# Kernel optimization log

Measured on AMD Instinct MI355X. Metric: run time of the kernel, lower is better.

Reference implementation:

```python
import jax, jax.numpy as jnp
import numpy as np

B, S, H, MODES = 16, 8192, 256, 16

def setup_inputs() -> dict:
    key = jax.random.key(0)
    k1, k2, k3 = jax.random.split(key, 3)
    x = jax.random.normal(k1, (B, S, H), dtype=jnp.float32)
    # complex weights ~ 0.02 * randn (real and imag parts kept as floats)
    w_real = jax.random.normal(k2, (H, H, MODES), dtype=jnp.float32) * 0.02
    w_imag = jax.random.normal(k3, (H, H, MODES), dtype=jnp.float32) * 0.02
    return {"x": x, "w_real": w_real, "w_imag": w_imag}

def reference(x, w_real, w_imag):
    batch, seq_len, hidden = x.shape
    x_ft = jnp.fft.rfft(x, axis=1)                      # [B, F, H] complex64, F = S//2 + 1
    m = min(MODES, x_ft.shape[1])
    w = (w_real + 1j * w_imag)[:, :, :m]                # [H, K, m]
    # batched complex matmul over the kept modes (replaces per-mode loop)
    out_modes = jnp.einsum('bmh,hkm->bmk', x_ft[:, :m, :], w)
    out_ft = jnp.zeros_like(x_ft).at[:, :m, :].set(out_modes)
    y = jnp.fft.irfft(out_ft, n=seq_len, axis=1)        # [B, S, H] float32
    return jax.nn.gelu(y, approximate=False)            # torch nn.GELU default = exact erf
```

## Files before the change

kernel.cpp:

```cpp
#include <hip/hip_runtime.h>
#include <math.h>

#define BB 16
#define SS 8192
#define HH 256
#define MM 16
#define NV 2049
#define VC 8
#define CPB 4
#define DNC 65
#define SCH 16
#define SNC 129


__device__ __forceinline__ void gl_lds16(const float* g, float* l) {
    __builtin_amdgcn_global_load_lds(
        (const __attribute__((address_space(1))) void*)g,
        (__attribute__((address_space(3))) void*)l, 16, 0, 0);
}

__global__ __launch_bounds__(256) void k_twiddle(float* __restrict__ T) {
    int idx = blockIdx.x * 256 + threadIdx.x;
    if (idx >= NV * MM) return;
    int v = idx >> 4, k = idx & 15;
    int r = (k * v) & (SS - 1);
    float th = (float)r * (6.28318530717958647692f / (float)SS);
    float sn, cn;
    sincosf(th, &sn, &cn);
    T[v * 32 + 2 * k]     = cn;
    T[v * 32 + 2 * k + 1] = sn;
}

__global__ __launch_bounds__(256) void k_wt(const float* __restrict__ wr,
                                            const float* __restrict__ wi,
                                            float* __restrict__ Wtr,
                                            float* __restrict__ Wti) {
    __shared__ float lds[4096 + 256];
    const int h = blockIdx.x, t = threadIdx.x;
    const float* src = (blockIdx.y == 0 ? wr : wi) + (size_t)h * 4096;
    float* dst = (blockIdx.y == 0 ? Wtr : Wti);
#pragma unroll
    for (int j = 0; j < 16; j++) {
        int i = j * 256 + t;
        lds[i + (i >> 4)] = src[i];
    }
    __syncthreads();
#pragma unroll
    for (int m = 0; m < 16; m++) {
        int i = t * 16 + m;
        dst[(size_t)m * (HH * HH) + (size_t)h * HH + t] = lds[i + (i >> 4)];
    }
}

__device__ __forceinline__ float fast_gelu(float y) {
    float x  = fabsf(y) * 0.70710678118654752f;
    float t  = __builtin_amdgcn_rcpf(fmaf(0.3275911f, x, 1.0f));
    float e  = __expf(-x * x);
    float p  = fmaf(fmaf(fmaf(fmaf(1.061405429f, t, -1.453152027f), t,
                   1.421413741f), t, -0.284496736f), t, 0.254829592f) * t;
    float erfabs = fmaf(-p, e, 1.0f);
    return fmaf(0.5f * fabsf(y), erfabs, 0.5f * y);
}

__global__ __launch_bounds__(256) void k_dft(const float* __restrict__ x,
                                             const float* __restrict__ T,
                                             float* __restrict__ Xp) {
    const int b = blockIdx.y, bx = blockIdx.x, t = threadIdx.x;
    const int w = t >> 6;
    const float* xb = x + (size_t)b * SS * HH;

    float cs[MM], sn[MM];
#pragma unroll
    for (int k = 0; k < MM; k++) { cs[k] = 0.f; sn[k] = 0.f; }

    __shared__ float lds[2][4 * VC * HH];

    if (bx == 64) {
        float x0 = xb[t];
        float x2 = xb[(size_t)(SS / 2) * HH + t];
#pragma unroll
        for (int j = 0; j < 8; j++) {
            cs[2 * j]     = x0 + x2;
            cs[2 * j + 1] = x0 - x2;
        }
    } else {
        const int c0 = bx * CPB;

        auto stage = [&](int c, int buf) {
            int v0 = 1 + VC * c;
            const float* bases[4] = {
                xb + (size_t)v0 * HH,
                xb + (size_t)(SS / 2 - v0 - (VC - 1)) * HH,
                xb + (size_t)(SS / 2 + v0) * HH,
                xb + (size_t)(SS - v0 - (VC - 1)) * HH };
#pragma unroll
            for (int s = 0; s < 4; s++)
#pragma unroll
                for (int q = 0; q < 2; q++)
                    gl_lds16(bases[s] + q * 1024 + t * 4,
                             &lds[buf][s * 2048 + q * 1024 + w * 256]);
        };

        auto compute = [&](int c, int buf) {
            int v0 = 1 + VC * c;
            const float* L = &lds[buf][0];
#pragma unroll
            for (int i = 0; i < VC; i++) {
                int v = v0 + i;
                float x0 = L[0 * 2048 + i * 256 + t];
                float x2 = L[1 * 2048 + (VC - 1 - i) * 256 + t];
                float x3 = L[2 * 2048 + i * 256 + t];
                float x1 = L[3 * 2048 + (VC - 1 - i) * 256 + t];
                float hf = (v == SS / 4) ? 0.5f : 1.0f;
                float u = (x0 + x1) * hf, d = (x0 - x1) * hf;
                float ww = (x2 + x3) * hf, e = (x3 - x2) * hf;
                float upw = u + ww, umw = u - ww, dpe = d + e, dme = d - e;
                const float4* tw4 = (const float4*)(T + (size_t)v * 32);
#pragma unroll
                for (int j = 0; j < 8; j++) {
                    float4 tt = tw4[j];
                    cs[2 * j]     = fmaf(tt.x, upw, cs[2 * j]);
                    sn[2 * j]     = fmaf(tt.y, dpe, sn[2 * j]);
                    cs[2 * j + 1] = fmaf(tt.z, umw, cs[2 * j + 1]);
                    sn[2 * j + 1] = fmaf(tt.w, dme, sn[2 * j + 1]);
                }
            }
        };

        stage(c0, 0);
        for (int j = 0; j < CPB; j++) {
            if (j < CPB - 1) {
                stage(c0 + j + 1, (j + 1) & 1);
                asm volatile("s_waitcnt vmcnt(8)" ::: "memory");
            } else {
                asm volatile("s_waitcnt vmcnt(0)" ::: "memory");
            }
            __builtin_amdgcn_sched_barrier(0);
            __builtin_amdgcn_s_barrier();
            compute(c0 + j, j & 1);
            __builtin_amdgcn_s_barrier();
        }
    }

    size_t base = ((size_t)(b * DNC + bx) * MM) * (2 * HH) + t;
#pragma unroll
    for (int k = 0; k < MM; k++) {
        Xp[base + (size_t)k * (2 * HH)]      = cs[k];
        Xp[base + (size_t)k * (2 * HH) + HH] = sn[k];
    }
}

__global__ __launch_bounds__(256) void k_reduce(const float* __restrict__ Xp,
                                                float* __restrict__ Xs) {
    const int t = blockIdx.x * 256 + threadIdx.x;
    const int INNER = MM * 2 * HH;
    int idx4 = t * 4;
    int inner = idx4 & (INNER - 1);
    int b = idx4 >> 13;
    const float* src = Xp + ((size_t)b * DNC) * INNER + inner;
    float4 s = make_float4(0.f, 0.f, 0.f, 0.f);
#pragma unroll 5
    for (int p = 0; p < DNC; p++) {
        float4 v = *(const float4*)(src + (size_t)p * INNER);
        s.x += v.x; s.y += v.y; s.z += v.z; s.w += v.w;
    }
    *(float4*)(Xs + idx4) = s;
}

__global__ __launch_bounds__(256) void k_mix2(const float* __restrict__ Xs,
                                              const float* __restrict__ Wtr,
                                              const float* __restrict__ Wti,
                                              float* __restrict__ AB) {
    const int m = blockIdx.x, b = blockIdx.y, t = threadIdx.x;
    __shared__ float xr_s[HH], xs_s[HH];
    size_t xbase = (((size_t)b * MM + m) * 2) * HH;
    xr_s[t] = Xs[xbase + t];
    xs_s[t] = Xs[xbase + HH + t];
    __syncthreads();

    const float* wr_m = Wtr + (size_t)m * (HH * HH);
    const float* wi_m = Wti + (size_t)m * (HH * HH);
    float re = 0.f, im = 0.f;
#pragma unroll 8
    for (int h = 0; h < HH; h++) {
        float a  = wr_m[(size_t)h * HH + t];
        float bw = wi_m[(size_t)h * HH + t];
        float xr = xr_s[h];
        float xs = xs_s[h];
        re = fmaf(xr, a, re);  re = fmaf(xs, bw, re);
        im = fmaf(xr, bw, im); im = fmaf(-xs, a, im);
    }
    float scale = (m == 0 ? 1.f : 2.f) / (float)SS;
    size_t o = (((size_t)b * MM + m) * 2) * HH + t;
    AB[o]      = scale * re;
    AB[o + HH] = -scale * im;
}

__global__ __launch_bounds__(256) void k_synth(const float* __restrict__ AB,
                                               const float* __restrict__ T,
                                               float* __restrict__ out) {
    const int c = blockIdx.x, b = blockIdx.y, h = threadIdx.x;
    float a[MM], bc[MM];
#pragma unroll
    for (int k = 0; k < MM; k++) {
        size_t o = (((size_t)b * MM + k) * 2) * HH + h;
        a[k]  = AB[o];
        bc[k] = AB[o + HH];
    }
    const int nv = (c == SNC - 1) ? 1 : SCH;
    const int v0 = c * SCH;
    float* ob = out + (size_t)b * SS * HH + h;

#pragma unroll 2
    for (int i = 0; i < nv; i++) {
        int v = v0 + i;
        const float4* tw4 = (const float4*)(T + (size_t)v * 32);
        float Pe = 0.f, Po = 0.f, Qe = 0.f, Qo = 0.f;
#pragma unroll
        for (int j = 0; j < 8; j++) {
            float4 t = tw4[j];
            Pe = fmaf(a[2 * j],      t.x, Pe);
            Qe = fmaf(bc[2 * j],     t.y, Qe);
            Po = fmaf(a[2 * j + 1],  t.z, Po);
            Qo = fmaf(bc[2 * j + 1], t.w, Qo);
        }
        float Pp = Pe + Po, Pm = Pe - Po, Qp = Qe + Qo, Qm = Qe - Qo;
        ob[(size_t)v * HH]                        = fast_gelu(Pp + Qp);
        ob[(size_t)(SS / 2 - v) * HH]             = fast_gelu(Pm - Qm);
        ob[(size_t)(SS / 2 + v) * HH]             = fast_gelu(Pm + Qm);
        ob[(size_t)((SS - v) & (SS - 1)) * HH]    = fast_gelu(Pp - Qp);
    }
}

extern "C" void kernel_launch(void* const* d_in, const int* in_sizes, int n_in,
                              void* d_out, int out_size, void* d_ws, size_t ws_size,
                              hipStream_t stream) {
    const float* x   = (const float*)d_in[0];
    const float* w_r = (const float*)d_in[1];
    const float* w_i = (const float*)d_in[2];
    float* out = (float*)d_out;
    float* ws  = (float*)d_ws;

    float* T   = ws;
    float* AB  = ws + 262144;
    float* Xs  = ws + 393216;
    float* Xp  = out;
    float* Wtr = out + (size_t)16 * 1024 * 1024;
    float* Wti = out + (size_t)17 * 1024 * 1024;

    hipLaunchKernelGGL(k_twiddle, dim3((NV * MM + 255) / 256), dim3(256), 0, stream, T);
    hipLaunchKernelGGL(k_wt,     dim3(HH, 2), dim3(256), 0, stream, w_r, w_i, Wtr, Wti);
    hipLaunchKernelGGL(k_dft,    dim3(DNC, BB), dim3(256), 0, stream, x, T, Xp);
    hipLaunchKernelGGL(k_reduce, dim3(BB * MM * 2 * HH / 1024), dim3(256), 0, stream, Xp, Xs);
    hipLaunchKernelGGL(k_mix2,   dim3(MM, BB), dim3(256), 0, stream, Xs, Wtr, Wti, AB);
    hipLaunchKernelGGL(k_synth,  dim3(SNC, BB), dim3(256), 0, stream, AB, T, out);
}
```

Baseline: 117.0 us.

## Fuse precompute kernels, fold partial reduce into mix, triple-buffer DFT loads

Merges the twiddle and weight-transpose kernels into a single launch, and moves the partial-sum reduction into the mode-mixing kernel so the separate reduce kernel and its intermediate buffer go away. The DFT kernel switches to smaller chunks (VC 4) with more chunks per block and a three-deep LDS ring buffer, which halves the number of partial blocks per batch. The intent is to cut launch overhead and intermediate traffic. The trade-off is fewer DFT blocks (33x16), which lowers parallelism, and a mix kernel that now does a strided partial sum itself.

After: 111.2 us. -4.9%, faster.

```diff
diff --git a/kernel.cpp b/kernel.cpp
--- a/kernel.cpp
+++ b/kernel.cpp
@@ -6,9 +6,9 @@
 #define HH 256
 #define MM 16
 #define NV 2049
-#define VC 8
-#define CPB 4
-#define DNC 65
+#define VC 4
+#define CPB 16
+#define DNC 33
 #define SCH 16
 #define SNC 129
 
@@ -19,36 +19,39 @@
         (__attribute__((address_space(3))) void*)l, 16, 0, 0);
 }
 
-__global__ __launch_bounds__(256) void k_twiddle(float* __restrict__ T) {
-    int idx = blockIdx.x * 256 + threadIdx.x;
-    if (idx >= NV * MM) return;
-    int v = idx >> 4, k = idx & 15;
-    int r = (k * v) & (SS - 1);
-    float th = (float)r * (6.28318530717958647692f / (float)SS);
-    float sn, cn;
-    sincosf(th, &sn, &cn);
-    T[v * 32 + 2 * k]     = cn;
-    T[v * 32 + 2 * k + 1] = sn;
-}
-
-__global__ __launch_bounds__(256) void k_wt(const float* __restrict__ wr,
-                                            const float* __restrict__ wi,
-                                            float* __restrict__ Wtr,
-                                            float* __restrict__ Wti) {
-    __shared__ float lds[4096 + 256];
-    const int h = blockIdx.x, t = threadIdx.x;
-    const float* src = (blockIdx.y == 0 ? wr : wi) + (size_t)h * 4096;
-    float* dst = (blockIdx.y == 0 ? Wtr : Wti);
-#pragma unroll
-    for (int j = 0; j < 16; j++) {
-        int i = j * 256 + t;
-        lds[i + (i >> 4)] = src[i];
-    }
-    __syncthreads();
-#pragma unroll
-    for (int m = 0; m < 16; m++) {
-        int i = t * 16 + m;
-        dst[(size_t)m * (HH * HH) + (size_t)h * HH + t] = lds[i + (i >> 4)];
+__global__ __launch_bounds__(256) void k_pre(const float* __restrict__ wr,
+                                             const float* __restrict__ wi,
+                                             float* __restrict__ T,
+                                             float* __restrict__ Wtr,
+                                             float* __restrict__ Wti) {
+    const int t = threadIdx.x;
+    if (blockIdx.x < 129) {
+        int idx = blockIdx.x * 256 + t;
+        if (idx >= NV * MM) return;
+        int v = idx >> 4, k = idx & 15;
+        int r = (k * v) & (SS - 1);
+        float th = (float)r * (6.28318530717958647692f / (float)SS);
+        float sn, cn;
+        sincosf(th, &sn, &cn);
+        T[v * 32 + 2 * k]     = cn;
+        T[v * 32 + 2 * k + 1] = sn;
+    } else {
+        __shared__ float lds[4096 + 256];
+        int bid = blockIdx.x - 129;
+        int h = bid & 255, y = bid >> 8;
+        const float* src = (y == 0 ? wr : wi) + (size_t)h * 4096;
+        float* dst = (y == 0 ? Wtr : Wti);
+#pragma unroll
+        for (int j = 0; j < 16; j++) {
+            int i = j * 256 + t;
+            lds[i + (i >> 4)] = src[i];
+        }
+        __syncthreads();
+#pragma unroll
+        for (int m = 0; m < 16; m++) {
+            int i = t * 16 + m;
+            dst[(size_t)m * (HH * HH) + (size_t)h * HH + t] = lds[i + (i >> 4)];
+        }
     }
 }
 
@@ -73,9 +76,9 @@
 #pragma unroll
     for (int k = 0; k < MM; k++) { cs[k] = 0.f; sn[k] = 0.f; }
 
-    __shared__ float lds[2][4 * VC * HH];
-
-    if (bx == 64) {
+    __shared__ float lds[3][4 * VC * HH];
+
+    if (bx == 32) {
         float x0 = xb[t];
         float x2 = xb[(size_t)(SS / 2) * HH + t];
 #pragma unroll
@@ -95,10 +98,7 @@
                 xb + (size_t)(SS - v0 - (VC - 1)) * HH };
 #pragma unroll
             for (int s = 0; s < 4; s++)
-#pragma unroll
-                for (int q = 0; q < 2; q++)
-                    gl_lds16(bases[s] + q * 1024 + t * 4,
-                             &lds[buf][s * 2048 + q * 1024 + w * 256]);
+                gl_lds16(bases[s] + t * 4, &lds[buf][s * 1024 + w * 256]);
         };
 
         auto compute = [&](int c, int buf) {
@@ -107,10 +107,10 @@
 #pragma unroll
             for (int i = 0; i < VC; i++) {
                 int v = v0 + i;
-                float x0 = L[0 * 2048 + i * 256 + t];
-                float x2 = L[1 * 2048 + (VC - 1 - i) * 256 + t];
-                float x3 = L[2 * 2048 + i * 256 + t];
-                float x1 = L[3 * 2048 + (VC - 1 - i) * 256 + t];
+                float x0 = L[0 * 1024 + i * 256 + t];
+                float x2 = L[1 * 1024 + (VC - 1 - i) * 256 + t];
+                float x3 = L[2 * 1024 + i * 256 + t];
+                float x1 = L[3 * 1024 + (VC - 1 - i) * 256 + t];
                 float hf = (v == SS / 4) ? 0.5f : 1.0f;
                 float u = (x0 + x1) * hf, d = (x0 - x1) * hf;
                 float ww = (x2 + x3) * hf, e = (x3 - x2) * hf;
@@ -128,16 +128,19 @@
         };
 
         stage(c0, 0);
+        stage(c0 + 1, 1);
         for (int j = 0; j < CPB; j++) {
-            if (j < CPB - 1) {
-                stage(c0 + j + 1, (j + 1) & 1);
+            if (j + 2 < CPB) {
+                stage(c0 + j + 2, (j + 2) % 3);
                 asm volatile("s_waitcnt vmcnt(8)" ::: "memory");
+            } else if (j + 1 < CPB) {
+                asm volatile("s_waitcnt vmcnt(4)" ::: "memory");
             } else {
                 asm volatile("s_waitcnt vmcnt(0)" ::: "memory");
             }
             __builtin_amdgcn_sched_barrier(0);
             __builtin_amdgcn_s_barrier();
-            compute(c0 + j, j & 1);
+            compute(c0 + j, j % 3);
             __builtin_amdgcn_s_barrier();
         }
     }
@@ -150,32 +153,23 @@
     }
 }
 
-__global__ __launch_bounds__(256) void k_reduce(const float* __restrict__ Xp,
-                                                float* __restrict__ Xs) {
-    const int t = blockIdx.x * 256 + threadIdx.x;
-    const int INNER = MM * 2 * HH;
-    int idx4 = t * 4;
-    int inner = idx4 & (INNER - 1);
-    int b = idx4 >> 13;
-    const float* src = Xp + ((size_t)b * DNC) * INNER + inner;
-    float4 s = make_float4(0.f, 0.f, 0.f, 0.f);
-#pragma unroll 5
-    for (int p = 0; p < DNC; p++) {
-        float4 v = *(const float4*)(src + (size_t)p * INNER);
-        s.x += v.x; s.y += v.y; s.z += v.z; s.w += v.w;
-    }
-    *(float4*)(Xs + idx4) = s;
-}
-
-__global__ __launch_bounds__(256) void k_mix2(const float* __restrict__ Xs,
-                                              const float* __restrict__ Wtr,
-                                              const float* __restrict__ Wti,
-                                              float* __restrict__ AB) {
+__global__ __launch_bounds__(256) void k_mix(const float* __restrict__ Xp,
+                                             const float* __restrict__ Wtr,
+                                             const float* __restrict__ Wti,
+                                             float* __restrict__ AB) {
     const int m = blockIdx.x, b = blockIdx.y, t = threadIdx.x;
     __shared__ float xr_s[HH], xs_s[HH];
-    size_t xbase = (((size_t)b * MM + m) * 2) * HH;
-    xr_s[t] = Xs[xbase + t];
-    xs_s[t] = Xs[xbase + HH + t];
+
+    float s0 = 0.f, s1 = 0.f;
+    size_t base = (((size_t)b * DNC) * MM + m) * (2 * HH) + t;
+    const size_t pstride = (size_t)MM * 2 * HH;
+#pragma unroll 4
+    for (int p = 0; p < DNC; p++) {
+        s0 += Xp[base + (size_t)p * pstride];
+        s1 += Xp[base + (size_t)p * pstride + HH];
+    }
+    xr_s[t] = s0;
+    xs_s[t] = s1;
     __syncthreads();
 
     const float* wr_m = Wtr + (size_t)m * (HH * HH);
@@ -243,15 +237,12 @@
 
     float* T   = ws;
     float* AB  = ws + 262144;
-    float* Xs  = ws + 393216;
     float* Xp  = out;
     float* Wtr = out + (size_t)16 * 1024 * 1024;
     float* Wti = out + (size_t)17 * 1024 * 1024;
 
-    hipLaunchKernelGGL(k_twiddle, dim3((NV * MM + 255) / 256), dim3(256), 0, stream, T);
-    hipLaunchKernelGGL(k_wt,     dim3(HH, 2), dim3(256), 0, stream, w_r, w_i, Wtr, Wti);
-    hipLaunchKernelGGL(k_dft,    dim3(DNC, BB), dim3(256), 0, stream, x, T, Xp);
-    hipLaunchKernelGGL(k_reduce, dim3(BB * MM * 2 * HH / 1024), dim3(256), 0, stream, Xp, Xs);
-    hipLaunchKernelGGL(k_mix2,   dim3(MM, BB), dim3(256), 0, stream, Xs, Wtr, Wti, AB);
-    hipLaunchKernelGGL(k_synth,  dim3(SNC, BB), dim3(256), 0, stream, AB, T, out);
-}
+    hipLaunchKernelGGL(k_pre,   dim3(641), dim3(256), 0, stream, w_r, w_i, T, Wtr, Wti);
+    hipLaunchKernelGGL(k_dft,   dim3(DNC, BB), dim3(256), 0, stream, x, T, Xp);
+    hipLaunchKernelGGL(k_mix,   dim3(MM, BB), dim3(256), 0, stream, Xp, Wtr, Wti, AB);
+    hipLaunchKernelGGL(k_synth, dim3(SNC, BB), dim3(256), 0, stream, AB, T, out);
+}
```
